# Optimization experiments

Measured on AMD Instinct MI355X. Metric: run time of the kernel, lower is better.

The kernel has to match this reference:

```python
import jax, jax.numpy as jnp
import numpy as np

V, E, H1, H2, B, T = 50000, 256, 512, 512, 512, 80

def setup_inputs() -> dict:
    key = jax.random.key(0)
    ks = jax.random.split(key, 10)
    s = lambda fan: 1.0 / np.sqrt(fan)
    return {
        "tokens": jax.random.randint(ks[0], (B, T), 0, V),
        "emb": jax.random.normal(ks[1], (V, E), jnp.float32) * 0.05,
        "W1": jax.random.normal(ks[2], (E, 4 * H1), jnp.float32) * s(E),
        "U1": jax.random.normal(ks[3], (H1, 4 * H1), jnp.float32) * s(H1),
        "b1": jnp.zeros((4 * H1,), jnp.float32),
        "W2": jax.random.normal(ks[4], (H1, 4 * H2), jnp.float32) * s(H1),
        "U2": jax.random.normal(ks[5], (H2, 4 * H2), jnp.float32) * s(H2),
        "b2": jnp.zeros((4 * H2,), jnp.float32),
        "Wfc": jax.random.normal(ks[6], (H2, 1), jnp.float32) * s(H2),
        "bfc": jnp.zeros((1,), jnp.float32),
    }

def _lstm_step(x, h, c, W, U, b):
    # z: [B, 4H] in Keras gate order i, f, g(cell), o
    z = x @ W + h @ U + b
    i, f, g, o = jnp.split(z, 4, axis=-1)
    c_new = jax.nn.sigmoid(f) * c + jax.nn.sigmoid(i) * jnp.tanh(g)
    h_new = jax.nn.sigmoid(o) * jnp.tanh(c_new)
    return h_new, c_new

def reference(tokens, emb, W1, U1, b1, W2, U2, b2, Wfc, bfc):
    X = emb[tokens]                    # [B, T, E]
    Xt = jnp.swapaxes(X, 0, 1)         # [T, B, E] for scan over time
    Bsz = tokens.shape[0]
    init = (jnp.zeros((Bsz, H1), X.dtype), jnp.zeros((Bsz, H1), X.dtype),
            jnp.zeros((Bsz, H2), X.dtype), jnp.zeros((Bsz, H2), X.dtype))

    def step(carry, x):
        h1, c1, h2, c2 = carry
        h1, c1 = _lstm_step(x, h1, c1, W1, U1, b1)
        h2, c2 = _lstm_step(h1, h2, c2, W2, U2, b2)
        return (h1, c1, h2, c2), None

    (h1, c1, h2, c2), _ = jax.lax.scan(step, init, Xt)
    # Dense(1) on last-step layer-2 output, then sigmoid (dropout inactive at inference)
    return jax.nn.sigmoid(h2 @ Wfc + bfc)   # [B, 1]
```

## Files before the change

### kernel.cpp

```cpp
#include <hip/hip_runtime.h>
#include <hip/hip_bf16.h>

typedef __bf16  bf16x8 __attribute__((ext_vector_type(8)));
typedef float   f32x4  __attribute__((ext_vector_type(4)));

#define GLOAD16_C(gptr, lptr) \
  __builtin_amdgcn_global_load_lds((const __attribute__((address_space(1))) void*)(gptr), \
                                   (__attribute__((address_space(3))) void*)(lptr), 16, 0, 0)
#define GLOAD16_H(gptr, lptr) \
  __builtin_amdgcn_global_load_lds((const __attribute__((address_space(1))) void*)(gptr), \
                                   (__attribute__((address_space(3))) void*)(lptr), 16, 0, 0x1)

#define WAIT_VM10  asm volatile("s_waitcnt vmcnt(10)" ::: "memory")
#define WAIT_VM8   asm volatile("s_waitcnt vmcnt(8)"  ::: "memory")
#define WAIT_VM6   asm volatile("s_waitcnt vmcnt(6)"  ::: "memory")
#define WAIT_VM4   asm volatile("s_waitcnt vmcnt(4)"  ::: "memory")
#define WAIT_VM2   asm volatile("s_waitcnt vmcnt(2)"  ::: "memory")
#define WAIT_VM0   asm volatile("s_waitcnt vmcnt(0)"  ::: "memory")

__device__ __forceinline__ void wait_vm_chunks(int n) {
  if      (n <= 0) WAIT_VM0;
  else if (n == 1) WAIT_VM2;
  else if (n == 2) WAIT_VM4;
  else if (n == 3) WAIT_VM6;
  else if (n == 4) WAIT_VM8;
  else             WAIT_VM10;
}
__device__ __forceinline__ void wait_lgkm_n(int n) {
  if      (n <= 0) asm volatile("s_waitcnt lgkmcnt(0)" ::: "memory");
  else if (n <= 2) asm volatile("s_waitcnt lgkmcnt(2)" ::: "memory");
  else             asm volatile("s_waitcnt lgkmcnt(6)" ::: "memory");
}

__device__ __forceinline__ float sigm(float x)  { return 1.0f / (1.0f + __expf(-x)); }
__device__ __forceinline__ float tanhp(float x) { return 2.0f / (1.0f + __expf(-2.0f * x)) - 1.0f; }

__device__ __forceinline__ unsigned int coh_load(const unsigned int* p) {
  unsigned int v;
  asm volatile("global_load_dword %0, %1, off sc0 sc1\n\ts_waitcnt vmcnt(0)"
               : "=v"(v) : "v"(p) : "memory");
  return v;
}
__device__ __forceinline__ int coh_load_i(const int* p) {
  int v;
  asm volatile("global_load_dword %0, %1, off sc0 sc1\n\ts_waitcnt vmcnt(0)"
               : "=v"(v) : "v"(p) : "memory");
  return v;
}
__device__ __forceinline__ void coh_store16(void* p, bf16x8 v) {
  f32x4 f = *(f32x4*)&v;
  asm volatile("global_store_dwordx4 %0, %1, off sc0 sc1" :: "v"(p), "v"(f) : "memory");
}
__device__ __forceinline__ void flag_store(int* fp, int v) {
  asm volatile("global_store_dword %0, %1, off sc0 sc1" :: "v"(fp), "v"(v) : "memory");
}

#define TSTEPS 80
#define BATCH  512
#define EDIM   256
#define HDIM   512
#define K2     1024
#define K1     768
#define NCH    16
#define D_SLOTS 12
#define SLOT_BYTES 524544
#define RING_OFF 65536
#define EPI_OFF  131072
#define EPI_STR  24
#define LDS_BYTES 137216

struct Params {
  const __hip_bfloat16* Wz1t;
  const __hip_bfloat16* Wz2t;
  const float* bz1;
  const float* bz2;
  const __hip_bfloat16* Xall;
  char* h1base;
  char* h2base;
  int* flags;
  const float* Wfc; const float* bfc;
  float* out;
};


__global__ __launch_bounds__(256) void prep_weights(
    const float* __restrict__ W1, const float* __restrict__ U1, const float* __restrict__ b1,
    const float* __restrict__ W2, const float* __restrict__ U2, const float* __restrict__ b2,
    __hip_bfloat16* __restrict__ Wz1t, __hip_bfloat16* __restrict__ Wz2t,
    float* __restrict__ bz1, float* __restrict__ bz2) {
  long idx = (long)blockIdx.x * 256 + threadIdx.x;
  const long n1 = 2048L * K1, n2 = 2048L * K2;
  if (idx < n1) {
    int n = (int)(idx / K1), k = (int)(idx % K1);
    int col = ((n >> 4) & 3) * 512 + (n >> 6) * 16 + (n & 15);
    float v = (k < 256) ? W1[(size_t)k * 2048 + col] : U1[(size_t)(k - 256) * 2048 + col];
    Wz1t[idx] = __float2bfloat16(v);
  } else if (idx < n1 + n2) {
    long r = idx - n1;
    int n = (int)(r / K2), k = (int)(r % K2);
    int col = ((n >> 4) & 3) * 512 + (n >> 6) * 16 + (n & 15);
    float v = (k < 512) ? W2[(size_t)k * 2048 + col] : U2[(size_t)(k - 512) * 2048 + col];
    Wz2t[r] = __float2bfloat16(v);
  } else if (idx < n1 + n2 + 2048) {
    int n = (int)(idx - (n1 + n2));
    bz1[n] = b1[((n >> 4) & 3) * 512 + (n >> 6) * 16 + (n & 15)];
  } else if (idx < n1 + n2 + 4096) {
    int n = (int)(idx - (n1 + n2 + 2048));
    bz2[n] = b2[((n >> 4) & 3) * 512 + (n >> 6) * 16 + (n & 15)];
  }
}

__global__ __launch_bounds__(256) void prep_gather(
    const int* __restrict__ tokens, const float* __restrict__ emb,
    __hip_bfloat16* __restrict__ Xall, float4* __restrict__ zp, int zn) {
  int idx = blockIdx.x * 256 + threadIdx.x;
  if (idx < zn) zp[idx] = make_float4(0.f, 0.f, 0.f, 0.f);
  int e  = (idx & 63) * 4;
  int rb = idx >> 6;
  int t  = rb >> 9;
  int b  = rb & 511;
  int tok = tokens[b * TSTEPS + t];
  const float4 v = *(const float4*)&emb[(size_t)tok * EDIM + e];
  __hip_bfloat16* o = Xall + (size_t)rb * EDIM + e;
  o[0] = __float2bfloat16(v.x); o[1] = __float2bfloat16(v.y);
  o[2] = __float2bfloat16(v.z); o[3] = __float2bfloat16(v.w);
}


__device__ __forceinline__ void gate_wave(const int* flags, int base1, int t1,
                                          int base2, int t2, int lane) {
  const int idx = lane & 31;
  const int* fp = flags + (((lane < 32) ? base1 : base2) + idx) * 4;
  const int tgt = (lane < 32) ? t1 : t2;
  for (;;) {
    int v = coh_load_i(fp);
    if (__ballot(v >= tgt) == ~0ull) break;
    __builtin_amdgcn_s_sleep(2);
  }
}

template<int K0, int LEN, int STRIDE, bool COH>
__device__ __forceinline__ void run_part(
    const __hip_bfloat16* __restrict__ Asrc, int m0, int w, int lane,
    __hip_bfloat16* __restrict__ ring, const __hip_bfloat16* __restrict__ BsL,
    const bf16x8 (&breg)[NCH][4], const int (&aoff)[2], const int (&boff)[4],
    f32x4 (&acc)[2][4]) {
  auto stage = [&](int kc) {
#pragma unroll
    for (int it = 0; it < 2; ++it) {
      const int gbase = w * 128 + it * 64;
      const int g   = gbase + lane;
      const int row = g >> 2;
      const int gc  = (g & 3) ^ ((row >> 1) & 3);
      __hip_bfloat16* lp = ring + (kc & 7) * 4096 + gbase * 8;
      const __hip_bfloat16* gp = Asrc + (size_t)(m0 + row) * STRIDE + (kc - K0) * 32 + gc * 8;
      if (COH) GLOAD16_H(gp, lp); else GLOAD16_C(gp, lp);
    }
  };
#pragma unroll
  for (int f = 0; f < 6; ++f) stage(K0 + f);

  bf16x8 af[2][2], bf[2][4];
  wait_vm_chunks(5);
#pragma unroll
  for (int mi = 0; mi < 2; ++mi)
    af[0][mi] = *(const bf16x8*)(ring + (K0 & 7) * 4096 + aoff[mi]);
  if (K0 >= NCH)
#pragma unroll
    for (int g = 0; g < 4; ++g)
      bf[0][g] = *(const bf16x8*)(BsL + (K0 - NCH) * 2048 + boff[g]);

#pragma unroll
  for (int i = 0; i < LEN; ++i) {
    const int kc  = K0 + i;
    const int cur = i & 1, nxt = cur ^ 1;
    if (i + 1 < LEN) {
      wait_vm_chunks(LEN - 2 - i < 4 ? LEN - 2 - i : 4);
      const int kn = kc + 1;
#pragma unroll
      for (int mi = 0; mi < 2; ++mi)
        af[nxt][mi] = *(const bf16x8*)(ring + (kn & 7) * 4096 + aoff[mi]);
      if (kn >= NCH) {
#pragma unroll
        for (int g = 0; g < 4; ++g)
          bf[nxt][g] = *(const bf16x8*)(BsL + (kn - NCH) * 2048 + boff[g]);
        wait_lgkm_n(6);
      } else {
        wait_lgkm_n(2);
      }
      if (i + 6 < LEN) stage(kc + 6);
    } else {
      wait_lgkm_n(0);
    }
#pragma unroll
    for (int mi = 0; mi < 2; ++mi)
#pragma unroll
      for (int g = 0; g < 4; ++g)
        acc[mi][g] = __builtin_amdgcn_mfma_f32_16x16x32_bf16(
            af[cur][mi], (kc < NCH ? breg[kc][g] : bf[cur][g]), acc[mi][g], 0, 0, 0);
  }
}

template<bool Z2>
__device__ __forceinline__ void role_loop(const Params& p, char* smem, int tid,
                                          int grp, int ntile) {
  constexpr int K   = Z2 ? K2 : K1;
  constexpr int NC  = K / 32;
  const int lane = tid & 63;
  const int w    = tid >> 6;
  const int q    = lane >> 4;
  const int m16  = lane & 15;
  const int m0   = grp * 128;
  const int n0   = ntile * 64;

  __hip_bfloat16* BsL  = (__hip_bfloat16*)smem;
  __hip_bfloat16* ring = (__hip_bfloat16*)(smem + RING_OFF);
  __hip_bfloat16* epi  = (__hip_bfloat16*)(smem + EPI_OFF);

  const __hip_bfloat16* Bg = (Z2 ? p.Wz2t : p.Wz1t) + (size_t)n0 * K;

  bf16x8 breg[NCH][4];
#pragma unroll
  for (int kc = 0; kc < NCH; ++kc)
#pragma unroll
    for (int g = 0; g < 4; ++g)
      breg[kc][g] = *(const bf16x8*)(Bg + (size_t)(g * 16 + m16) * K + kc * 32 + q * 8);

  for (int it0 = tid; it0 < (NC - NCH) * 256; it0 += 256) {
    int cid = it0 >> 8, gg = it0 & 255;
    int r = gg >> 2, c8 = gg & 3;
    int sw = c8 ^ ((r >> 1) & 3);
    *(bf16x8*)(BsL + cid * 2048 + r * 32 + sw * 8) =
        *(const bf16x8*)(Bg + (size_t)r * K + (NCH + cid) * 32 + c8 * 8);
  }
  const float* bias = Z2 ? p.bz2 : p.bz1;
  float bz[4];
#pragma unroll
  for (int g = 0; g < 4; ++g) bz[g] = bias[n0 + g * 16 + m16];

  const int swz = (q ^ ((m16 >> 1) & 3)) * 8;
  int aoff[2], boff[4];
#pragma unroll
  for (int mi = 0; mi < 2; ++mi) aoff[mi] = (w * 32 + mi * 16 + m16) * 32 + swz;
#pragma unroll
  for (int g = 0; g < 4; ++g)    boff[g]  = (g * 16 + m16) * 32 + swz;

  float cst[2][4] = {{0.f,0.f,0.f,0.f},{0.f,0.f,0.f,0.f}};
  const int fself = (Z2 ? 128 : 0) + grp * 32 + ntile;
  const int jbase = ntile * 16;
  __syncthreads();

  if (Z2) {
    if (w == 0) gate_wave(p.flags, grp * 32, 1, grp * 32, 1, lane);
    __syncthreads();
  }

  for (int s = 0; s < TSTEPS; ++s) {
    const int sl = s % D_SLOTS, slp = (s + D_SLOTS - 1) % D_SLOTS;
    const __hip_bfloat16* Aa = Z2
        ? (const __hip_bfloat16*)(p.h1base + (size_t)sl * SLOT_BYTES)
        : p.Xall + (size_t)s * BATCH * EDIM;
    const __hip_bfloat16* Ab = Z2
        ? (const __hip_bfloat16*)(p.h2base + (size_t)slp * SLOT_BYTES)
        : (const __hip_bfloat16*)(p.h1base + (size_t)slp * SLOT_BYTES);
    __hip_bfloat16* hout = (__hip_bfloat16*)
        ((Z2 ? p.h2base : p.h1base) + (size_t)sl * SLOT_BYTES);

    f32x4 acc[2][4];
#pragma unroll
    for (int mi = 0; mi < 2; ++mi)
#pragma unroll
      for (int g = 0; g < 4; ++g)
        acc[mi][g] = (f32x4){bz[g], bz[g], bz[g], bz[g]};

    if (Z2) run_part<0, 16, 512, true >(Aa, m0, w, lane, ring, BsL, breg, aoff, boff, acc);
    else    run_part<0,  8, 256, false>(Aa, m0, w, lane, ring, BsL, breg, aoff, boff, acc);

    if (w == 0) {
      if (Z2) gate_wave(p.flags, 128 + grp * 32, s, 128 + grp * 32, s, lane);
      else    gate_wave(p.flags, grp * 32, s, 128 + grp * 32, s - (D_SLOTS - 1), lane);
      if ((s & 7) == 0) __builtin_amdgcn_fence(__ATOMIC_ACQUIRE, "agent");
    }
    __syncthreads();
    if (Z2) run_part<16, 16, 512, true>(Ab, m0, w, lane, ring, BsL, breg, aoff, boff, acc);
    else    run_part< 8, 16, 512, true>(Ab, m0, w, lane, ring, BsL, breg, aoff, boff, acc);

#pragma unroll
    for (int mi = 0; mi < 2; ++mi)
#pragma unroll
      for (int rr = 0; rr < 4; ++rr) {
        const float zi = acc[mi][0][rr], zf = acc[mi][1][rr];
        const float zg = acc[mi][2][rr], zo = acc[mi][3][rr];
        const float cn = sigm(zf) * cst[mi][rr] + sigm(zi) * tanhp(zg);
        cst[mi][rr] = cn;
        epi[(w * 32 + mi * 16 + q * 4 + rr) * EPI_STR + m16] = __float2bfloat16(sigm(zo) * tanhp(cn));
      }
    __syncthreads();
    {
      const int r = tid >> 1, hf = tid & 1;
      bf16x8 hv = *(const bf16x8*)(epi + r * EPI_STR + hf * 8);
      coh_store16(hout + (size_t)(m0 + r) * HDIM + jbase + hf * 8, hv);
    }
    if (Z2 && w == 0 && s + 1 < TSTEPS)
      gate_wave(p.flags, grp * 32, s + 2, grp * 32, s + 2, lane);
    WAIT_VM0;
    __syncthreads();
    if (tid == 0) flag_store(p.flags + fself * 4, s + 1);
  }
}

__global__ __launch_bounds__(256, 1) void lstm_seq(Params p) {
  extern __shared__ char smem[];
  const int tid = threadIdx.x;
  const bool z2  = ((blockIdx.x & 1) == 0);
  const int grp  = (blockIdx.x >> 1) & 3;
  const int ntile = blockIdx.x >> 3;

  if (z2) role_loop<true>(p, smem, tid, grp, ntile);
  else    role_loop<false>(p, smem, tid, grp, ntile);

  const int lane = tid & 63, w = tid >> 6;
  if (w == 0) {
    const int g2 = blockIdx.x >> 6;
    gate_wave(p.flags, 128 + g2 * 32, TSTEPS, 128 + g2 * 32, TSTEPS, lane);
  }
  __syncthreads();
  if (w < 2) {
    const int row = blockIdx.x * 2 + w;
    const unsigned int* hp = (const unsigned int*)
        (p.h2base + (size_t)((TSTEPS - 1) % D_SLOTS) * SLOT_BYTES) + (size_t)row * (HDIM / 2);
    float sum = 0.f;
#pragma unroll
    for (int cc = 0; cc < 4; ++cc) {
      unsigned int d = coh_load(hp + lane * 4 + cc);
      union { unsigned int ui; float f; } lo, hi;
      lo.ui = d << 16; hi.ui = d & 0xffff0000u;
      sum += lo.f * p.Wfc[(lane * 4 + cc) * 2] + hi.f * p.Wfc[(lane * 4 + cc) * 2 + 1];
    }
#pragma unroll
    for (int o = 32; o > 0; o >>= 1) sum += __shfl_down(sum, o, 64);
    if (lane == 0) p.out[row] = sigm(sum + p.bfc[0]);
  }
}


extern "C" void kernel_launch(void* const* d_in, const int* in_sizes, int n_in,
                              void* d_out, int out_size, void* d_ws, size_t ws_size,
                              hipStream_t stream) {
  const int*   tokens = (const int*)d_in[0];
  const float* emb = (const float*)d_in[1];
  const float* W1  = (const float*)d_in[2];
  const float* U1  = (const float*)d_in[3];
  const float* b1  = (const float*)d_in[4];
  const float* W2  = (const float*)d_in[5];
  const float* U2  = (const float*)d_in[6];
  const float* b2  = (const float*)d_in[7];
  const float* Wfc = (const float*)d_in[8];
  const float* bfc = (const float*)d_in[9];

  char* ws = (char*)d_ws;
  size_t off = 0;
  auto alloc = [&](size_t bytes) {
    char* r = ws + off;
    off += (bytes + 255) & ~(size_t)255;
    return r;
  };
  __hip_bfloat16* Wz1t = (__hip_bfloat16*)alloc(2048UL * K1 * 2);
  __hip_bfloat16* Wz2t = (__hip_bfloat16*)alloc(2048UL * K2 * 2);
  float* bz1 = (float*)alloc(2048 * 4);
  float* bz2 = (float*)alloc(2048 * 4);
  __hip_bfloat16* Xall = (__hip_bfloat16*)alloc((size_t)TSTEPS * BATCH * EDIM * 2);
  const size_t state_bytes = 24UL * SLOT_BYTES + 4096;
  char* state = alloc(state_bytes);

  Params prm;
  prm.h1base = state;
  prm.h2base = state + 12UL * SLOT_BYTES;
  prm.flags  = (int*)(state + 24UL * SLOT_BYTES);

  prep_weights<<<dim3(14352), dim3(256), 0, stream>>>(W1, U1, b1, W2, U2, b2, Wz1t, Wz2t, bz1, bz2);
  prep_gather<<<dim3(10240), dim3(256), 0, stream>>>(tokens, emb, Xall,
                                                     (float4*)state, (int)(state_bytes / 16));

  hipFuncSetAttribute((const void*)lstm_seq,
                      hipFuncAttributeMaxDynamicSharedMemorySize, LDS_BYTES);

  prm.Wz1t = Wz1t; prm.Wz2t = Wz2t; prm.bz1 = bz1; prm.bz2 = bz2;
  prm.Xall = Xall;
  prm.Wfc = Wfc; prm.bfc = bfc;
  prm.out = (float*)d_out;

  lstm_seq<<<dim3(256), dim3(256), LDS_BYTES, stream>>>(prm);
}
```

Before: 696.0 us.

## Prefetch next timestep's input-part tiles before the step-end barrier and flag publish

The first six k-chunks of the next timestep's input operand (embeddings for layer 1, h1 for layer 2) are now issued into the LDS ring at the end of the current step, before the barrier and flag store, instead of at the start of the next step. The A-part of run_part gets a PREFILLED template flag that skips its own prologue loads. The goal is to hide global-load latency behind the step-boundary synchronisation. In exchange, layer 2 now has every wave poll the h1 flags before prefetching, and it drops the full vmcnt(0) wait before publishing its flag, so it relies on the flag store's ordering for h2 visibility.

```diff
diff --git a/kernel.cpp b/kernel.cpp
--- a/kernel.cpp
+++ b/kernel.cpp
@@ -11,6 +11,7 @@
   __builtin_amdgcn_global_load_lds((const __attribute__((address_space(1))) void*)(gptr), \
                                    (__attribute__((address_space(3))) void*)(lptr), 16, 0, 0x1)
 
+#define WAIT_VM12  asm volatile("s_waitcnt vmcnt(12)" ::: "memory")
 #define WAIT_VM10  asm volatile("s_waitcnt vmcnt(10)" ::: "memory")
 #define WAIT_VM8   asm volatile("s_waitcnt vmcnt(8)"  ::: "memory")
 #define WAIT_VM6   asm volatile("s_waitcnt vmcnt(6)"  ::: "memory")
@@ -139,7 +140,25 @@
   }
 }
 
-template<int K0, int LEN, int STRIDE, bool COH>
+template<int STRIDE, bool COH>
+__device__ __forceinline__ void prefill6(const __hip_bfloat16* __restrict__ A,
+    int m0, int w, int lane, __hip_bfloat16* __restrict__ ring) {
+#pragma unroll
+  for (int f = 0; f < 6; ++f) {
+#pragma unroll
+    for (int it = 0; it < 2; ++it) {
+      const int gbase = w * 128 + it * 64;
+      const int g   = gbase + lane;
+      const int row = g >> 2;
+      const int gc  = (g & 3) ^ ((row >> 1) & 3);
+      __hip_bfloat16* lp = ring + f * 4096 + gbase * 8;
+      const __hip_bfloat16* gp = A + (size_t)(m0 + row) * STRIDE + f * 32 + gc * 8;
+      if (COH) GLOAD16_H(gp, lp); else GLOAD16_C(gp, lp);
+    }
+  }
+}
+
+template<int K0, int LEN, int STRIDE, bool COH, bool PREFILLED>
 __device__ __forceinline__ void run_part(
     const __hip_bfloat16* __restrict__ Asrc, int m0, int w, int lane,
     __hip_bfloat16* __restrict__ ring, const __hip_bfloat16* __restrict__ BsL,
@@ -157,8 +176,10 @@
       if (COH) GLOAD16_H(gp, lp); else GLOAD16_C(gp, lp);
     }
   };
-#pragma unroll
-  for (int f = 0; f < 6; ++f) stage(K0 + f);
+  if (!PREFILLED) {
+#pragma unroll
+    for (int f = 0; f < 6; ++f) stage(K0 + f);
+  }
 
   bf16x8 af[2][2], bf[2][4];
   wait_vm_chunks(5);
@@ -253,6 +274,9 @@
   if (Z2) {
     if (w == 0) gate_wave(p.flags, grp * 32, 1, grp * 32, 1, lane);
     __syncthreads();
+    prefill6<HDIM, true>((const __hip_bfloat16*)p.h1base, m0, w, lane, ring);
+  } else {
+    prefill6<EDIM, false>(p.Xall, m0, w, lane, ring);
   }
 
   for (int s = 0; s < TSTEPS; ++s) {
@@ -273,8 +297,8 @@
       for (int g = 0; g < 4; ++g)
         acc[mi][g] = (f32x4){bz[g], bz[g], bz[g], bz[g]};
 
-    if (Z2) run_part<0, 16, 512, true >(Aa, m0, w, lane, ring, BsL, breg, aoff, boff, acc);
-    else    run_part<0,  8, 256, false>(Aa, m0, w, lane, ring, BsL, breg, aoff, boff, acc);
+    if (Z2) run_part<0, 16, 512, true,  true>(Aa, m0, w, lane, ring, BsL, breg, aoff, boff, acc);
+    else    run_part<0,  8, 256, false, true>(Aa, m0, w, lane, ring, BsL, breg, aoff, boff, acc);
 
     if (w == 0) {
       if (Z2) gate_wave(p.flags, 128 + grp * 32, s, 128 + grp * 32, s, lane);
@@ -282,8 +306,8 @@
       if ((s & 7) == 0) __builtin_amdgcn_fence(__ATOMIC_ACQUIRE, "agent");
     }
     __syncthreads();
-    if (Z2) run_part<16, 16, 512, true>(Ab, m0, w, lane, ring, BsL, breg, aoff, boff, acc);
-    else    run_part< 8, 16, 512, true>(Ab, m0, w, lane, ring, BsL, breg, aoff, boff, acc);
+    if (Z2) run_part<16, 16, 512, true, false>(Ab, m0, w, lane, ring, BsL, breg, aoff, boff, acc);
+    else    run_part< 8, 16, 512, true, false>(Ab, m0, w, lane, ring, BsL, breg, aoff, boff, acc);
 
 #pragma unroll
     for (int mi = 0; mi < 2; ++mi)
@@ -301,11 +325,25 @@
       bf16x8 hv = *(const bf16x8*)(epi + r * EPI_STR + hf * 8);
       coh_store16(hout + (size_t)(m0 + r) * HDIM + jbase + hf * 8, hv);
     }
-    if (Z2 && w == 0 && s + 1 < TSTEPS)
-      gate_wave(p.flags, grp * 32, s + 2, grp * 32, s + 2, lane);
-    WAIT_VM0;
-    __syncthreads();
-    if (tid == 0) flag_store(p.flags + fself * 4, s + 1);
+
+    if (s + 1 < TSTEPS) {
+      if (Z2) {
+        gate_wave(p.flags, grp * 32, s + 2, grp * 32, s + 2, lane);
+        const __hip_bfloat16* An = (const __hip_bfloat16*)
+            (p.h1base + (size_t)((s + 1) % D_SLOTS) * SLOT_BYTES);
+        prefill6<HDIM, true>(An, m0, w, lane, ring);
+      } else {
+        const __hip_bfloat16* An = p.Xall + (size_t)(s + 1) * BATCH * EDIM;
+        prefill6<EDIM, false>(An, m0, w, lane, ring);
+        WAIT_VM12;
+      }
+      __syncthreads();
+      if (tid == 0) flag_store(p.flags + fself * 4, s + 1);
+    } else {
+      WAIT_VM0;
+      __syncthreads();
+      if (tid == 0) flag_store(p.flags + fself * 4, s + 1);
+    }
   }
 }
 
```

New measurement: 722.7 us. 3.8% more time.

## Load A fragments directly into registers with deep prefetch, drop LDS ring

Applied to the files above, without the earlier changes.

Replaces the global-to-LDS ring staging of activation tiles with direct per-lane global dwordx4 loads into a 10-deep register queue, waiting on vmcnt before each MFMA step. It also cuts the register-resident weight chunks from 16 to 12 so the extra A registers fit, and shrinks LDS. The aim is to remove LDS write/read traffic and the barriers tied to it on the latency-critical recurrent path. In exchange, global loads are no longer cooperatively coalesced through LDS, register pressure rises, and more B chunks are now read from LDS.

```diff
diff --git a/kernel.cpp b/kernel.cpp
--- a/kernel.cpp
+++ b/kernel.cpp
@@ -4,36 +4,32 @@
 typedef __bf16  bf16x8 __attribute__((ext_vector_type(8)));
 typedef float   f32x4  __attribute__((ext_vector_type(4)));
 
-#define GLOAD16_C(gptr, lptr) \
-  __builtin_amdgcn_global_load_lds((const __attribute__((address_space(1))) void*)(gptr), \
-                                   (__attribute__((address_space(3))) void*)(lptr), 16, 0, 0)
-#define GLOAD16_H(gptr, lptr) \
-  __builtin_amdgcn_global_load_lds((const __attribute__((address_space(1))) void*)(gptr), \
-                                   (__attribute__((address_space(3))) void*)(lptr), 16, 0, 0x1)
-
-#define WAIT_VM10  asm volatile("s_waitcnt vmcnt(10)" ::: "memory")
-#define WAIT_VM8   asm volatile("s_waitcnt vmcnt(8)"  ::: "memory")
-#define WAIT_VM6   asm volatile("s_waitcnt vmcnt(6)"  ::: "memory")
-#define WAIT_VM4   asm volatile("s_waitcnt vmcnt(4)"  ::: "memory")
-#define WAIT_VM2   asm volatile("s_waitcnt vmcnt(2)"  ::: "memory")
-#define WAIT_VM0   asm volatile("s_waitcnt vmcnt(0)"  ::: "memory")
-
-__device__ __forceinline__ void wait_vm_chunks(int n) {
-  if      (n <= 0) WAIT_VM0;
-  else if (n == 1) WAIT_VM2;
-  else if (n == 2) WAIT_VM4;
-  else if (n == 3) WAIT_VM6;
-  else if (n == 4) WAIT_VM8;
-  else             WAIT_VM10;
-}
-__device__ __forceinline__ void wait_lgkm_n(int n) {
-  if      (n <= 0) asm volatile("s_waitcnt lgkmcnt(0)" ::: "memory");
-  else if (n <= 2) asm volatile("s_waitcnt lgkmcnt(2)" ::: "memory");
-  else             asm volatile("s_waitcnt lgkmcnt(6)" ::: "memory");
-}
+__device__ __forceinline__ void wait_vm_n(int n) {
+  switch (n) {
+    case 0:  asm volatile("s_waitcnt vmcnt(0)"  ::: "memory"); break;
+    case 2:  asm volatile("s_waitcnt vmcnt(2)"  ::: "memory"); break;
+    case 4:  asm volatile("s_waitcnt vmcnt(4)"  ::: "memory"); break;
+    case 6:  asm volatile("s_waitcnt vmcnt(6)"  ::: "memory"); break;
+    case 8:  asm volatile("s_waitcnt vmcnt(8)"  ::: "memory"); break;
+    case 10: asm volatile("s_waitcnt vmcnt(10)" ::: "memory"); break;
+    case 12: asm volatile("s_waitcnt vmcnt(12)" ::: "memory"); break;
+    case 14: asm volatile("s_waitcnt vmcnt(14)" ::: "memory"); break;
+    case 16: asm volatile("s_waitcnt vmcnt(16)" ::: "memory"); break;
+    default: asm volatile("s_waitcnt vmcnt(18)" ::: "memory"); break;
+  }
+}
+#define WAIT_VM0 asm volatile("s_waitcnt vmcnt(0)" ::: "memory")
 
 __device__ __forceinline__ float sigm(float x)  { return 1.0f / (1.0f + __expf(-x)); }
 __device__ __forceinline__ float tanhp(float x) { return 2.0f / (1.0f + __expf(-2.0f * x)) - 1.0f; }
+
+template<bool COH>
+__device__ __forceinline__ bf16x8 gl16(const __hip_bfloat16* p) {
+  f32x4 v;
+  if (COH) asm volatile("global_load_dwordx4 %0, %1, off sc0" : "=v"(v) : "v"(p));
+  else     asm volatile("global_load_dwordx4 %0, %1, off"     : "=v"(v) : "v"(p));
+  return *(bf16x8*)&v;
+}
 
 __device__ __forceinline__ unsigned int coh_load(const unsigned int* p) {
   unsigned int v;
@@ -61,13 +57,13 @@
 #define HDIM   512
 #define K2     1024
 #define K1     768
-#define NCH    16
+#define NCH    12
+#define ADEPTH 10
 #define D_SLOTS 12
 #define SLOT_BYTES 524544
-#define RING_OFF 65536
-#define EPI_OFF  131072
+#define EPI_OFF  81920
 #define EPI_STR  24
-#define LDS_BYTES 137216
+#define LDS_BYTES 88064
 
 struct Params {
   const __hip_bfloat16* Wz1t;
@@ -142,62 +138,51 @@
 template<int K0, int LEN, int STRIDE, bool COH>
 __device__ __forceinline__ void run_part(
     const __hip_bfloat16* __restrict__ Asrc, int m0, int w, int lane,
-    __hip_bfloat16* __restrict__ ring, const __hip_bfloat16* __restrict__ BsL,
-    const bf16x8 (&breg)[NCH][4], const int (&aoff)[2], const int (&boff)[4],
+    const __hip_bfloat16* __restrict__ BsL,
+    const bf16x8 (&breg)[NCH][4], const int (&boff)[4],
     f32x4 (&acc)[2][4]) {
-  auto stage = [&](int kc) {
-#pragma unroll
-    for (int it = 0; it < 2; ++it) {
-      const int gbase = w * 128 + it * 64;
-      const int g   = gbase + lane;
-      const int row = g >> 2;
-      const int gc  = (g & 3) ^ ((row >> 1) & 3);
-      __hip_bfloat16* lp = ring + (kc & 7) * 4096 + gbase * 8;
-      const __hip_bfloat16* gp = Asrc + (size_t)(m0 + row) * STRIDE + (kc - K0) * 32 + gc * 8;
-      if (COH) GLOAD16_H(gp, lp); else GLOAD16_C(gp, lp);
-    }
-  };
-#pragma unroll
-  for (int f = 0; f < 6; ++f) stage(K0 + f);
-
-  bf16x8 af[2][2], bf[2][4];
-  wait_vm_chunks(5);
-#pragma unroll
-  for (int mi = 0; mi < 2; ++mi)
-    af[0][mi] = *(const bf16x8*)(ring + (K0 & 7) * 4096 + aoff[mi]);
-  if (K0 >= NCH)
+  const int q = lane >> 4, m16 = lane & 15;
+  const __hip_bfloat16* b0 = Asrc + (size_t)(m0 + w * 32 + m16) * STRIDE + q * 8;
+  const __hip_bfloat16* b1 = b0 + (size_t)16 * STRIDE;
+
+  bf16x8 af[ADEPTH][2];
+  bf16x8 bf[2][4];
+  constexpr int F = (ADEPTH < LEN) ? ADEPTH : LEN;
+#pragma unroll
+  for (int f = 0; f < F; ++f) {
+    af[f][0] = gl16<COH>(b0 + f * 32);
+    af[f][1] = gl16<COH>(b1 + f * 32);
+  }
+  if (K0 >= NCH) {
 #pragma unroll
     for (int g = 0; g < 4; ++g)
       bf[0][g] = *(const bf16x8*)(BsL + (K0 - NCH) * 2048 + boff[g]);
+  }
 
 #pragma unroll
   for (int i = 0; i < LEN; ++i) {
     const int kc  = K0 + i;
     const int cur = i & 1, nxt = cur ^ 1;
-    if (i + 1 < LEN) {
-      wait_vm_chunks(LEN - 2 - i < 4 ? LEN - 2 - i : 4);
-      const int kn = kc + 1;
-#pragma unroll
-      for (int mi = 0; mi < 2; ++mi)
-        af[nxt][mi] = *(const bf16x8*)(ring + (kn & 7) * 4096 + aoff[mi]);
-      if (kn >= NCH) {
-#pragma unroll
-        for (int g = 0; g < 4; ++g)
-          bf[nxt][g] = *(const bf16x8*)(BsL + (kn - NCH) * 2048 + boff[g]);
-        wait_lgkm_n(6);
-      } else {
-        wait_lgkm_n(2);
-      }
-      if (i + 6 < LEN) stage(kc + 6);
-    } else {
-      wait_lgkm_n(0);
+    if (i + 1 < LEN && kc + 1 >= NCH) {
+#pragma unroll
+      for (int g = 0; g < 4; ++g)
+        bf[nxt][g] = *(const bf16x8*)(BsL + (kc + 1 - NCH) * 2048 + boff[g]);
+    }
+    {
+      const int rem = LEN - 1 - i;
+      wait_vm_n(2 * (ADEPTH - 1 < rem ? ADEPTH - 1 : rem));
+      __builtin_amdgcn_sched_barrier(0);
     }
 #pragma unroll
     for (int mi = 0; mi < 2; ++mi)
 #pragma unroll
       for (int g = 0; g < 4; ++g)
         acc[mi][g] = __builtin_amdgcn_mfma_f32_16x16x32_bf16(
-            af[cur][mi], (kc < NCH ? breg[kc][g] : bf[cur][g]), acc[mi][g], 0, 0, 0);
+            af[i % ADEPTH][mi], (kc < NCH ? breg[kc][g] : bf[cur][g]), acc[mi][g], 0, 0, 0);
+    if (i + ADEPTH < LEN) {
+      af[i % ADEPTH][0] = gl16<COH>(b0 + (i + ADEPTH) * 32);
+      af[i % ADEPTH][1] = gl16<COH>(b1 + (i + ADEPTH) * 32);
+    }
   }
 }
 
@@ -214,7 +199,6 @@
   const int n0   = ntile * 64;
 
   __hip_bfloat16* BsL  = (__hip_bfloat16*)smem;
-  __hip_bfloat16* ring = (__hip_bfloat16*)(smem + RING_OFF);
   __hip_bfloat16* epi  = (__hip_bfloat16*)(smem + EPI_OFF);
 
   const __hip_bfloat16* Bg = (Z2 ? p.Wz2t : p.Wz1t) + (size_t)n0 * K;
@@ -239,11 +223,9 @@
   for (int g = 0; g < 4; ++g) bz[g] = bias[n0 + g * 16 + m16];
 
   const int swz = (q ^ ((m16 >> 1) & 3)) * 8;
-  int aoff[2], boff[4];
-#pragma unroll
-  for (int mi = 0; mi < 2; ++mi) aoff[mi] = (w * 32 + mi * 16 + m16) * 32 + swz;
-#pragma unroll
-  for (int g = 0; g < 4; ++g)    boff[g]  = (g * 16 + m16) * 32 + swz;
+  int boff[4];
+#pragma unroll
+  for (int g = 0; g < 4; ++g) boff[g] = (g * 16 + m16) * 32 + swz;
 
   float cst[2][4] = {{0.f,0.f,0.f,0.f},{0.f,0.f,0.f,0.f}};
   const int fself = (Z2 ? 128 : 0) + grp * 32 + ntile;
@@ -273,8 +255,8 @@
       for (int g = 0; g < 4; ++g)
         acc[mi][g] = (f32x4){bz[g], bz[g], bz[g], bz[g]};
 
-    if (Z2) run_part<0, 16, 512, true >(Aa, m0, w, lane, ring, BsL, breg, aoff, boff, acc);
-    else    run_part<0,  8, 256, false>(Aa, m0, w, lane, ring, BsL, breg, aoff, boff, acc);
+    if (Z2) run_part<0, 16, 512, true >(Aa, m0, w, lane, BsL, breg, boff, acc);
+    else    run_part<0,  8, 256, false>(Aa, m0, w, lane, BsL, breg, boff, acc);
 
     if (w == 0) {
       if (Z2) gate_wave(p.flags, 128 + grp * 32, s, 128 + grp * 32, s, lane);
@@ -282,8 +264,8 @@
       if ((s & 7) == 0) __builtin_amdgcn_fence(__ATOMIC_ACQUIRE, "agent");
     }
     __syncthreads();
-    if (Z2) run_part<16, 16, 512, true>(Ab, m0, w, lane, ring, BsL, breg, aoff, boff, acc);
-    else    run_part< 8, 16, 512, true>(Ab, m0, w, lane, ring, BsL, breg, aoff, boff, acc);
+    if (Z2) run_part<16, 16, 512, true>(Ab, m0, w, lane, BsL, breg, boff, acc);
+    else    run_part< 8, 16, 512, true>(Ab, m0, w, lane, BsL, breg, boff, acc);
 
 #pragma unroll
     for (int mi = 0; mi < 2; ++mi)
```

Result: slower. 973.5 us (+39.9%).

## Split K across wave pairs with LDS reduction in persistent LSTM kernel

Applied to the files above, without the earlier changes.

Doubles the block to 512 threads: each row-group of waves is split into two K-halves (even/odd 32-wide chunks), each holding half the register-resident weights and staging its own A chunks into a larger 12-slot ring. Partial accumulators from one half are written to a new LDS reduction buffer and summed by the other half, which then does the gate epilogue and the h store. This aims to shorten the per-step serial GEMM latency on the recurrent critical path and lower register pressure per wave. In exchange it adds extra barriers, an LDS round trip per step and more LDS use, and launch_bounds(512,2) may force register spills.

```diff
diff --git a/kernel.cpp b/kernel.cpp
--- a/kernel.cpp
+++ b/kernel.cpp
@@ -62,12 +62,15 @@
 #define K2     1024
 #define K1     768
 #define NCH    16
+#define NCHW   8
+#define RS     12
 #define D_SLOTS 12
 #define SLOT_BYTES 524544
 #define RING_OFF 65536
-#define EPI_OFF  131072
+#define RED_OFF  65536
+#define EPI_OFF  98304
 #define EPI_STR  24
-#define LDS_BYTES 137216
+#define LDS_BYTES 163840
 
 struct Params {
   const __hip_bfloat16* Wz1t;
@@ -141,54 +144,56 @@
 
 template<int K0, int LEN, int STRIDE, bool COH>
 __device__ __forceinline__ void run_part(
-    const __hip_bfloat16* __restrict__ Asrc, int m0, int w, int lane,
+    const __hip_bfloat16* __restrict__ Asrc, int m0, int wr, int wk, int lane,
     __hip_bfloat16* __restrict__ ring, const __hip_bfloat16* __restrict__ BsL,
-    const bf16x8 (&breg)[NCH][4], const int (&aoff)[2], const int (&boff)[4],
+    const bf16x8 (&breg)[NCHW][4], const int (&aoff)[2], const int (&boff)[4],
     f32x4 (&acc)[2][4]) {
-  auto stage = [&](int kc) {
+  constexpr int L = LEN / 2;
+  constexpr int FILLW = (L < 5) ? L : 5;
+  auto stage = [&](int i) {
+    const int so = ((K0 + 2 * i) % RS);
 #pragma unroll
     for (int it = 0; it < 2; ++it) {
-      const int gbase = w * 128 + it * 64;
+      const int gbase = wr * 128 + it * 64;
       const int g   = gbase + lane;
       const int row = g >> 2;
       const int gc  = (g & 3) ^ ((row >> 1) & 3);
-      __hip_bfloat16* lp = ring + (kc & 7) * 4096 + gbase * 8;
-      const __hip_bfloat16* gp = Asrc + (size_t)(m0 + row) * STRIDE + (kc - K0) * 32 + gc * 8;
+      __hip_bfloat16* lp = ring + (so + wk) * 4096 + gbase * 8;
+      const __hip_bfloat16* gp = Asrc + (size_t)(m0 + row) * STRIDE + (2 * i + wk) * 32 + gc * 8;
       if (COH) GLOAD16_H(gp, lp); else GLOAD16_C(gp, lp);
     }
   };
 #pragma unroll
-  for (int f = 0; f < 6; ++f) stage(K0 + f);
+  for (int f = 0; f < FILLW; ++f) stage(f);
 
   bf16x8 af[2][2], bf[2][4];
-  wait_vm_chunks(5);
+  wait_vm_chunks(FILLW - 1);
 #pragma unroll
   for (int mi = 0; mi < 2; ++mi)
-    af[0][mi] = *(const bf16x8*)(ring + (K0 & 7) * 4096 + aoff[mi]);
-  if (K0 >= NCH)
+    af[0][mi] = *(const bf16x8*)(ring + ((K0 % RS) + wk) * 4096 + aoff[mi]);
+  if (K0 + 1 >= NCH) {
 #pragma unroll
     for (int g = 0; g < 4; ++g)
-      bf[0][g] = *(const bf16x8*)(BsL + (K0 - NCH) * 2048 + boff[g]);
-
-#pragma unroll
-  for (int i = 0; i < LEN; ++i) {
-    const int kc  = K0 + i;
+      bf[0][g] = *(const bf16x8*)(BsL + (K0 + wk - NCH) * 2048 + boff[g]);
+  }
+
+#pragma unroll
+  for (int i = 0; i < L; ++i) {
     const int cur = i & 1, nxt = cur ^ 1;
-    if (i + 1 < LEN) {
-      wait_vm_chunks(LEN - 2 - i < 4 ? LEN - 2 - i : 4);
-      const int kn = kc + 1;
+    if (i + 1 < L) {
+      wait_vm_chunks(L - 2 - i < 3 ? L - 2 - i : 3);
 #pragma unroll
       for (int mi = 0; mi < 2; ++mi)
-        af[nxt][mi] = *(const bf16x8*)(ring + (kn & 7) * 4096 + aoff[mi]);
-      if (kn >= NCH) {
+        af[nxt][mi] = *(const bf16x8*)(ring + (((K0 + 2 * (i + 1)) % RS) + wk) * 4096 + aoff[mi]);
+      if (K0 + 2 * (i + 1) + 1 >= NCH) {
 #pragma unroll
         for (int g = 0; g < 4; ++g)
-          bf[nxt][g] = *(const bf16x8*)(BsL + (kn - NCH) * 2048 + boff[g]);
+          bf[nxt][g] = *(const bf16x8*)(BsL + (K0 + 2 * (i + 1) + wk - NCH) * 2048 + boff[g]);
         wait_lgkm_n(6);
       } else {
         wait_lgkm_n(2);
       }
-      if (i + 6 < LEN) stage(kc + 6);
+      if (i + FILLW < L) stage(i + FILLW);
     } else {
       wait_lgkm_n(0);
     }
@@ -197,7 +202,9 @@
 #pragma unroll
       for (int g = 0; g < 4; ++g)
         acc[mi][g] = __builtin_amdgcn_mfma_f32_16x16x32_bf16(
-            af[cur][mi], (kc < NCH ? breg[kc][g] : bf[cur][g]), acc[mi][g], 0, 0, 0);
+            af[cur][mi],
+            (K0 + 2 * i + 1 < NCH ? breg[((K0 >> 1) + i) & (NCHW - 1)][g] : bf[cur][g]),
+            acc[mi][g], 0, 0, 0);
   }
 }
 
@@ -208,6 +215,8 @@
   constexpr int NC  = K / 32;
   const int lane = tid & 63;
   const int w    = tid >> 6;
+  const int wk   = w & 1;
+  const int wr   = w >> 1;
   const int q    = lane >> 4;
   const int m16  = lane & 15;
   const int m0   = grp * 128;
@@ -219,14 +228,14 @@
 
   const __hip_bfloat16* Bg = (Z2 ? p.Wz2t : p.Wz1t) + (size_t)n0 * K;
 
-  bf16x8 breg[NCH][4];
-#pragma unroll
-  for (int kc = 0; kc < NCH; ++kc)
+  bf16x8 breg[NCHW][4];
+#pragma unroll
+  for (int j = 0; j < NCHW; ++j)
 #pragma unroll
     for (int g = 0; g < 4; ++g)
-      breg[kc][g] = *(const bf16x8*)(Bg + (size_t)(g * 16 + m16) * K + kc * 32 + q * 8);
-
-  for (int it0 = tid; it0 < (NC - NCH) * 256; it0 += 256) {
+      breg[j][g] = *(const bf16x8*)(Bg + (size_t)(g * 16 + m16) * K + (2 * j + wk) * 32 + q * 8);
+
+  for (int it0 = tid; it0 < (NC - NCH) * 256; it0 += 512) {
     int cid = it0 >> 8, gg = it0 & 255;
     int r = gg >> 2, c8 = gg & 3;
     int sw = c8 ^ ((r >> 1) & 3);
@@ -241,7 +250,7 @@
   const int swz = (q ^ ((m16 >> 1) & 3)) * 8;
   int aoff[2], boff[4];
 #pragma unroll
-  for (int mi = 0; mi < 2; ++mi) aoff[mi] = (w * 32 + mi * 16 + m16) * 32 + swz;
+  for (int mi = 0; mi < 2; ++mi) aoff[mi] = (wr * 32 + mi * 16 + m16) * 32 + swz;
 #pragma unroll
   for (int g = 0; g < 4; ++g)    boff[g]  = (g * 16 + m16) * 32 + swz;
 
@@ -270,11 +279,13 @@
 #pragma unroll
     for (int mi = 0; mi < 2; ++mi)
 #pragma unroll
-      for (int g = 0; g < 4; ++g)
-        acc[mi][g] = (f32x4){bz[g], bz[g], bz[g], bz[g]};
-
-    if (Z2) run_part<0, 16, 512, true >(Aa, m0, w, lane, ring, BsL, breg, aoff, boff, acc);
-    else    run_part<0,  8, 256, false>(Aa, m0, w, lane, ring, BsL, breg, aoff, boff, acc);
+      for (int g = 0; g < 4; ++g) {
+        const float b = wk ? bz[g] : 0.f;
+        acc[mi][g] = (f32x4){b, b, b, b};
+      }
+
+    if (Z2) run_part<0, 16, 512, true >(Aa, m0, wr, wk, lane, ring, BsL, breg, aoff, boff, acc);
+    else    run_part<0,  8, 256, false>(Aa, m0, wr, wk, lane, ring, BsL, breg, aoff, boff, acc);
 
     if (w == 0) {
       if (Z2) gate_wave(p.flags, 128 + grp * 32, s, 128 + grp * 32, s, lane);
@@ -282,22 +293,41 @@
       if ((s & 7) == 0) __builtin_amdgcn_fence(__ATOMIC_ACQUIRE, "agent");
     }
     __syncthreads();
-    if (Z2) run_part<16, 16, 512, true>(Ab, m0, w, lane, ring, BsL, breg, aoff, boff, acc);
-    else    run_part< 8, 16, 512, true>(Ab, m0, w, lane, ring, BsL, breg, aoff, boff, acc);
-
-#pragma unroll
-    for (int mi = 0; mi < 2; ++mi)
-#pragma unroll
-      for (int rr = 0; rr < 4; ++rr) {
-        const float zi = acc[mi][0][rr], zf = acc[mi][1][rr];
-        const float zg = acc[mi][2][rr], zo = acc[mi][3][rr];
-        const float cn = sigm(zf) * cst[mi][rr] + sigm(zi) * tanhp(zg);
-        cst[mi][rr] = cn;
-        epi[(w * 32 + mi * 16 + q * 4 + rr) * EPI_STR + m16] = __float2bfloat16(sigm(zo) * tanhp(cn));
-      }
-    __syncthreads();
-    {
-      const int r = tid >> 1, hf = tid & 1;
+    if (Z2) run_part<16, 16, 512, true>(Ab, m0, wr, wk, lane, ring, BsL, breg, aoff, boff, acc);
+    else    run_part< 8, 16, 512, true>(Ab, m0, wr, wk, lane, ring, BsL, breg, aoff, boff, acc);
+
+    __syncthreads();
+    if (!wk) {
+      float* red = (float*)(smem + RED_OFF);
+#pragma unroll
+      for (int mi = 0; mi < 2; ++mi)
+#pragma unroll
+        for (int g = 0; g < 4; ++g)
+          *(f32x4*)(red + wr * 2048 + (mi * 4 + g) * 256 + lane * 4) = acc[mi][g];
+    }
+    __syncthreads();
+    if (wk) {
+      const float* red = (const float*)(smem + RED_OFF);
+#pragma unroll
+      for (int mi = 0; mi < 2; ++mi)
+#pragma unroll
+        for (int g = 0; g < 4; ++g)
+          acc[mi][g] += *(const f32x4*)(red + wr * 2048 + (mi * 4 + g) * 256 + lane * 4);
+#pragma unroll
+      for (int mi = 0; mi < 2; ++mi)
+#pragma unroll
+        for (int rr = 0; rr < 4; ++rr) {
+          const float zi = acc[mi][0][rr], zf = acc[mi][1][rr];
+          const float zg = acc[mi][2][rr], zo = acc[mi][3][rr];
+          const float cn = sigm(zf) * cst[mi][rr] + sigm(zi) * tanhp(zg);
+          cst[mi][rr] = cn;
+          epi[(wr * 32 + mi * 16 + q * 4 + rr) * EPI_STR + m16] = __float2bfloat16(sigm(zo) * tanhp(cn));
+        }
+    }
+    __syncthreads();
+    if (wk) {
+      const int idx = wr * 64 + lane;
+      const int r = idx >> 1, hf = idx & 1;
       bf16x8 hv = *(const bf16x8*)(epi + r * EPI_STR + hf * 8);
       coh_store16(hout + (size_t)(m0 + r) * HDIM + jbase + hf * 8, hv);
     }
@@ -309,7 +339,7 @@
   }
 }
 
-__global__ __launch_bounds__(256, 1) void lstm_seq(Params p) {
+__global__ __launch_bounds__(512, 2) void lstm_seq(Params p) {
   extern __shared__ char smem[];
   const int tid = threadIdx.x;
   const bool z2  = ((blockIdx.x & 1) == 0);
@@ -390,5 +420,5 @@
   prm.Wfc = Wfc; prm.bfc = bfc;
   prm.out = (float*)d_out;
 
-  lstm_seq<<<dim3(256), dim3(256), LDS_BYTES, stream>>>(prm);
-}
+  lstm_seq<<<dim3(256), dim3(512), LDS_BYTES, stream>>>(prm);
+}
```

Result: slower. 783.9 us (+12.6%).
